# Performance work log

Hardware: AMD Instinct MI355X
Metric: run time of the kernel (lower is better)

Reference implementation:

```python
import jax, jax.numpy as jnp
import numpy as np

L = 44                      # num_lods
IMG = 178                   # output image side
HASH_SIZE = 1 << 10         # codebook_bitwidth = 10
PRIME = np.uint32(2654435761)
RES = np.round(16.0 * (128.0 / 16.0) ** (np.arange(L) / (L - 1.0))).astype(np.int32)
DENSE = (RES + 1) ** 2 <= HASH_SIZE            # dense level if it fits in 2^10 entries
SIZES = np.where(DENSE, (RES + 1) ** 2, HASH_SIZE).astype(np.int32)
OFFS = np.concatenate([[0], np.cumsum(SIZES)[:-1]]).astype(np.int32)
TOTAL = int(SIZES.sum())    # 38584 shared codebook entries (latent_dim = 1)


def setup_inputs() -> dict:
    key = jax.random.key(0)
    k = jax.random.split(key, 5)
    B, N = 16, IMG * IMG
    x = jax.random.uniform(k[0], (B, N, 2), dtype=jnp.float32)            # 2D coords in [0,1]
    codebook = 0.1 * jax.random.normal(k[1], (B, TOTAL, 1), jnp.float32)  # feature_std=0.1
    w1 = jax.random.normal(k[2], (B, 16, L), jnp.float32) / np.sqrt(L)
    w2 = jax.random.normal(k[3], (B, 16, 16), jnp.float32) / 4.0
    w3 = jax.random.normal(k[4], (B, 3, 16), jnp.float32) / 4.0
    return {"x": x, "codebook": codebook, "w1": w1, "w2": w2, "w3": w3}


def _grid_lookup(x, codebook):
    """Multi-LOD hashed 2D grid bilinear lookup. x:[B,N,2], codebook:[B,T,1] -> [B,N,L]."""
    B, N, _ = x.shape
    res_f = jnp.asarray(RES, jnp.float32)
    res_i = jnp.asarray(RES)
    scaled = x[:, :, None, :] * res_f[None, None, :, None]          # [B,N,L,2]
    base = jnp.floor(scaled)
    frac = scaled - base
    base = base.astype(jnp.int32)
    corners = jnp.array([[0, 0], [0, 1], [1, 0], [1, 1]], jnp.int32)  # [4,2]
    c = base[:, :, :, None, :] + corners[None, None, None]          # [B,N,L,4,2]
    c = jnp.minimum(c, res_i[None, None, :, None, None])
    cx, cy = c[..., 0], c[..., 1]
    dense_idx = cy * (res_i + 1)[None, None, :, None] + cx          # row-major dense index
    h = (cx.astype(jnp.uint32) ^ (cy.astype(jnp.uint32) * PRIME)) % jnp.uint32(HASH_SIZE)
    idx = jnp.where(jnp.asarray(DENSE)[None, None, :, None], dense_idx, h.astype(jnp.int32))
    idx = idx + jnp.asarray(OFFS)[None, None, :, None]              # [B,N,L,4] into shared table
    vals = jnp.take_along_axis(codebook[:, :, 0], idx.reshape(B, -1), axis=1).reshape(B, N, L, 4)
    fr = frac[:, :, :, None, :]                                     # [B,N,L,1,2]
    w = jnp.where(corners[None, None, None] == 1, fr, 1.0 - fr).prod(-1)  # bilinear wts [B,N,L,4]
    return (vals * w).sum(-1)                                       # [B,N,L]


def reference(x, codebook, w1, w2, w3):
    feats = _grid_lookup(x, codebook)                               # [B,N,44] ('cat' multiscale)
    h = jax.nn.relu(jnp.einsum('bnl,bhl->bnh', feats, w1))          # per-sample hypernet weights
    h = jax.nn.relu(jnp.einsum('bnh,bkh->bnk', h, w2))
    rgb = jax.nn.sigmoid(jnp.einsum('bnk,bck->bnc', h, w3))         # [B,N,3]
    return rgb.reshape(x.shape[0], IMG, IMG, 3)
```

## Files before the change

kernel.cpp:

```cpp
#include <hip/hip_runtime.h>
#include <math.h>

#define NLEV 44
#define NDENSE 15
#define IMG 178
#define NPTS (IMG*IMG)
#define HASH_SIZE 1024
#define PRIME 2654435761u
#define BLOCK 1024
#define PTS_PER_BLOCK (2*BLOCK)

typedef __attribute__((ext_vector_type(2))) float f32x2;

struct LevelParams {
    int res[NLEV];
    int offs[NLEV];
    int total;
};

#define PKFMA_S(acc, a, b) \
    asm("v_pk_fma_f32 %0, %1, %2, %0" : "+v"(acc) : "v"(a), "s"(b))

__global__ __launch_bounds__(1024) void transpose_w1(const float* __restrict__ w1,
                                                     float* __restrict__ w1t) {
    const int b = blockIdx.x;
    const int i = threadIdx.x;
    if (i < 16 * NLEV) {
        const int l = i >> 4, o = i & 15;
        w1t[(size_t)b * 16 * NLEV + i] = w1[(size_t)b * 16 * NLEV + o * NLEV + l];
    }
}

template<int L0, int CNT, bool TP>
__device__ __forceinline__ void dense_group(
    const LevelParams& lp, const float* __restrict__ sCB,
    const float* __restrict__ w1b,
    float2 xy0, float2 xy1, f32x2* __restrict__ h1a, f32x2* __restrict__ h1b)
{
    float v[2][CNT][4];
    float fr[2][CNT][2];
#pragma unroll
    for (int i = 0; i < CNT; ++i) {
        const int l = L0 + i;
        const int res = lp.res[l];
        const int st  = res + 1;
        const int off = lp.offs[l];
        const float rf = (float)res;
#pragma unroll
        for (int p = 0; p < 2; ++p) {
            const float2 xy = p ? xy1 : xy0;
            const float sx = xy.x * rf, sy = xy.y * rf;
            const int ix0 = (int)sx, iy0 = (int)sy;
            fr[p][i][0] = sx - (float)ix0;
            fr[p][i][1] = sy - (float)iy0;
            const int r0 = off + iy0 * st + ix0;
            v[p][i][0] = sCB[r0];
            v[p][i][1] = sCB[r0 + 1];
            v[p][i][2] = sCB[r0 + st];
            v[p][i][3] = sCB[r0 + st + 1];
        }
    }
#pragma unroll
    for (int i = 0; i < CNT; ++i) {
        const int l = L0 + i;
        f32x2 wlv[8];
        if constexpr (TP) {
            const f32x2* wp = (const f32x2*)(w1b + l * 16);
#pragma unroll
            for (int j = 0; j < 8; ++j) wlv[j] = wp[j];
        } else {
#pragma unroll
            for (int j = 0; j < 8; ++j) {
                wlv[j].x = w1b[(2 * j) * NLEV + l];
                wlv[j].y = w1b[(2 * j + 1) * NLEV + l];
            }
        }
#pragma unroll
        for (int p = 0; p < 2; ++p) {
            f32x2* h1 = p ? h1b : h1a;
            const float vx0 = fmaf(fr[p][i][0], v[p][i][1] - v[p][i][0], v[p][i][0]);
            const float vx1 = fmaf(fr[p][i][0], v[p][i][3] - v[p][i][2], v[p][i][2]);
            const float feat = fmaf(fr[p][i][1], vx1 - vx0, vx0);
            f32x2 f2; f2.x = feat; f2.y = feat;
#pragma unroll
            for (int j = 0; j < 8; ++j) PKFMA_S(h1[j], f2, wlv[j]);
        }
    }
}

template<int L0, int CNT, bool TP>
__device__ __forceinline__ void hash_group(
    const LevelParams& lp, const float* __restrict__ sCB,
    const float* __restrict__ w1b,
    float2 xy0, float2 xy1, f32x2* __restrict__ h1a, f32x2* __restrict__ h1b)
{
    float v[2][CNT][4];
    float fr[2][CNT][2];
#pragma unroll
    for (int i = 0; i < CNT; ++i) {
        const int l = L0 + i;
        const int off = lp.offs[l];
        const float rf = (float)lp.res[l];
#pragma unroll
        for (int p = 0; p < 2; ++p) {
            const float2 xy = p ? xy1 : xy0;
            const float sx = xy.x * rf, sy = xy.y * rf;
            const int ix0 = (int)sx, iy0 = (int)sy;
            fr[p][i][0] = sx - (float)ix0;
            fr[p][i][1] = sy - (float)iy0;
            const unsigned px0 = (unsigned)ix0, px1 = px0 + 1u;
            const unsigned py0 = (unsigned)iy0 * PRIME, py1 = py0 + PRIME;
            const int i00 = (int)((px0 ^ py0) & (HASH_SIZE - 1));
            const int i01 = (int)((px0 ^ py1) & (HASH_SIZE - 1));
            const int i10 = (int)((px1 ^ py0) & (HASH_SIZE - 1));
            const int i11 = (int)((px1 ^ py1) & (HASH_SIZE - 1));
            v[p][i][0] = sCB[off + i00];
            v[p][i][1] = sCB[off + i10];
            v[p][i][2] = sCB[off + i01];
            v[p][i][3] = sCB[off + i11];
        }
    }
#pragma unroll
    for (int i = 0; i < CNT; ++i) {
        const int l = L0 + i;
        f32x2 wlv[8];
        if constexpr (TP) {
            const f32x2* wp = (const f32x2*)(w1b + l * 16);
#pragma unroll
            for (int j = 0; j < 8; ++j) wlv[j] = wp[j];
        } else {
#pragma unroll
            for (int j = 0; j < 8; ++j) {
                wlv[j].x = w1b[(2 * j) * NLEV + l];
                wlv[j].y = w1b[(2 * j + 1) * NLEV + l];
            }
        }
#pragma unroll
        for (int p = 0; p < 2; ++p) {
            f32x2* h1 = p ? h1b : h1a;
            const float vx0 = fmaf(fr[p][i][0], v[p][i][1] - v[p][i][0], v[p][i][0]);
            const float vx1 = fmaf(fr[p][i][0], v[p][i][3] - v[p][i][2], v[p][i][2]);
            const float feat = fmaf(fr[p][i][1], vx1 - vx0, vx0);
            f32x2 f2; f2.x = feat; f2.y = feat;
#pragma unroll
            for (int j = 0; j < 8; ++j) PKFMA_S(h1[j], f2, wlv[j]);
        }
    }
}

template<bool TP>
__global__ __launch_bounds__(BLOCK) void shacira_kernel(
    const float* __restrict__ x, const float* __restrict__ codebook,
    const float* __restrict__ w1, const float* __restrict__ w1t,
    const float* __restrict__ w2, const float* __restrict__ w3,
    float* __restrict__ out, LevelParams lp)
{
    extern __shared__ float sCB[];
    const int total = lp.total;
    const int tid = threadIdx.x;
    const int b = blockIdx.y;

    {
        const float* cbg = codebook + (size_t)b * total;
        const float4* src = (const float4*)cbg;
        float4* dst = (float4*)sCB;
        const int n4 = total >> 2;
        for (int i = tid; i < n4; i += BLOCK) dst[i] = src[i];
        for (int i = (n4 << 2) + tid; i < total; i += BLOCK) sCB[i] = cbg[i];
    }
    __syncthreads();

    const float* w1b = TP ? (w1t + (size_t)b * 16 * NLEV) : (w1 + (size_t)b * 16 * NLEV);
    const float* w2b = w2 + (size_t)b * 256;
    const float* w3b = w3 + (size_t)b * 48;

    const int n0 = blockIdx.x * PTS_PER_BLOCK + tid;
    const int n1 = n0 + BLOCK;
    const bool valid0 = n0 < NPTS;
    const bool valid1 = n1 < NPTS;
    const float2* xg = (const float2*)x + (size_t)b * NPTS;
    float2 xy0 = valid0 ? xg[n0] : make_float2(0.f, 0.f);
    float2 xy1 = valid1 ? xg[n1] : make_float2(0.f, 0.f);

    f32x2 h1a[8], h1b[8];
#pragma unroll
    for (int j = 0; j < 8; ++j) {
        h1a[j].x = 0.f; h1a[j].y = 0.f;
        h1b[j].x = 0.f; h1b[j].y = 0.f;
    }

    dense_group<0, 4, TP>(lp, sCB, w1b, xy0, xy1, h1a, h1b);
    dense_group<4, 4, TP>(lp, sCB, w1b, xy0, xy1, h1a, h1b);
    dense_group<8, 4, TP>(lp, sCB, w1b, xy0, xy1, h1a, h1b);
    dense_group<12, 3, TP>(lp, sCB, w1b, xy0, xy1, h1a, h1b);
    hash_group<15, 4, TP>(lp, sCB, w1b, xy0, xy1, h1a, h1b);
    hash_group<19, 4, TP>(lp, sCB, w1b, xy0, xy1, h1a, h1b);
    hash_group<23, 4, TP>(lp, sCB, w1b, xy0, xy1, h1a, h1b);
    hash_group<27, 4, TP>(lp, sCB, w1b, xy0, xy1, h1a, h1b);
    hash_group<31, 4, TP>(lp, sCB, w1b, xy0, xy1, h1a, h1b);
    hash_group<35, 4, TP>(lp, sCB, w1b, xy0, xy1, h1a, h1b);
    hash_group<39, 4, TP>(lp, sCB, w1b, xy0, xy1, h1a, h1b);
    hash_group<43, 1, TP>(lp, sCB, w1b, xy0, xy1, h1a, h1b);

    auto mlp = [&](f32x2* h1, int n, bool valid) {
        if (!valid) return;
#pragma unroll
        for (int j = 0; j < 8; ++j) {
            h1[j].x = fmaxf(h1[j].x, 0.f);
            h1[j].y = fmaxf(h1[j].y, 0.f);
        }
        float h2[16];
#pragma unroll
        for (int o = 0; o < 16; ++o) {
            const f32x2* w2v = (const f32x2*)(w2b + o * 16);
            f32x2 acc; acc.x = 0.f; acc.y = 0.f;
#pragma unroll
            for (int k = 0; k < 8; ++k) PKFMA_S(acc, h1[k], w2v[k]);
            h2[o] = fmaxf(acc.x + acc.y, 0.f);
        }
        f32x2 h2v[8];
#pragma unroll
        for (int j = 0; j < 8; ++j) { h2v[j].x = h2[2 * j]; h2v[j].y = h2[2 * j + 1]; }
        float rgb[3];
#pragma unroll
        for (int c = 0; c < 3; ++c) {
            const f32x2* w3v = (const f32x2*)(w3b + c * 16);
            f32x2 acc; acc.x = 0.f; acc.y = 0.f;
#pragma unroll
            for (int k = 0; k < 8; ++k) PKFMA_S(acc, h2v[k], w3v[k]);
            rgb[c] = 1.f / (1.f + expf(-(acc.x + acc.y)));
        }
        float* op = out + ((size_t)b * NPTS + n) * 3;
        op[0] = rgb[0]; op[1] = rgb[1]; op[2] = rgb[2];
    };
    mlp(h1a, n0, valid0);
    mlp(h1b, n1, valid1);
}

extern "C" void kernel_launch(void* const* d_in, const int* in_sizes, int n_in,
                              void* d_out, int out_size, void* d_ws, size_t ws_size,
                              hipStream_t stream) {
    const float* x        = (const float*)d_in[0];
    const float* codebook = (const float*)d_in[1];
    const float* w1       = (const float*)d_in[2];
    const float* w2       = (const float*)d_in[3];
    const float* w3       = (const float*)d_in[4];
    float* out = (float*)d_out;

    const int B = in_sizes[0] / (NPTS * 2);

    LevelParams lp;
    int off = 0;
    for (int l = 0; l < NLEV; ++l) {
        const double r = 16.0 * pow(128.0 / 16.0, (double)l / (double)(NLEV - 1));
        const int res = (int)llrint(r);
        lp.res[l] = res;
        lp.offs[l] = off;
        const int sz = ((long long)(res + 1) * (res + 1) <= HASH_SIZE)
                           ? (res + 1) * (res + 1) : HASH_SIZE;
        off += sz;
    }
    lp.total = off;

    const size_t smemBytes = (size_t)lp.total * 4;
    const size_t w1tBytes = (size_t)B * 16 * NLEV * 4;
    const bool tp = ws_size >= w1tBytes;

    dim3 grid((NPTS + PTS_PER_BLOCK - 1) / PTS_PER_BLOCK, B);
    if (tp) {
        transpose_w1<<<dim3(B), dim3(1024), 0, stream>>>(w1, (float*)d_ws);
        hipFuncSetAttribute((const void*)shacira_kernel<true>,
                            hipFuncAttributeMaxDynamicSharedMemorySize, (int)smemBytes);
        shacira_kernel<true><<<grid, dim3(BLOCK), smemBytes, stream>>>(
            x, codebook, w1, (const float*)d_ws, w2, w3, out, lp);
    } else {
        hipFuncSetAttribute((const void*)shacira_kernel<false>,
                            hipFuncAttributeMaxDynamicSharedMemorySize, (int)smemBytes);
        shacira_kernel<false><<<grid, dim3(BLOCK), smemBytes, stream>>>(
            x, codebook, w1, (const float*)0, w2, w3, out, lp);
    }
}
```

Before: 39.98 us.

## Keep only first 36 levels in LDS, gather last 8 hash levels from global

Shrinks the per-block shared-memory codebook copy to the first 36 levels and reads the last 8 hashed levels directly from global memory (served by L2). The aim is to cut the staging copy and LDS footprint, which could allow more resident blocks per CU. In exchange, the random gathers for the finest levels become global loads with much higher latency than LDS reads.

```diff
diff --git a/kernel.cpp b/kernel.cpp
--- a/kernel.cpp
+++ b/kernel.cpp
@@ -3,6 +3,7 @@
 
 #define NLEV 44
 #define NDENSE 15
+#define NLDS 36
 #define IMG 178
 #define NPTS (IMG*IMG)
 #define HASH_SIZE 1024
@@ -16,6 +17,7 @@
     int res[NLEV];
     int offs[NLEV];
     int total;
+    int ldsTotal;
 };
 
 #define PKFMA_S(acc, a, b) \
@@ -28,6 +30,40 @@
     if (i < 16 * NLEV) {
         const int l = i >> 4, o = i & 15;
         w1t[(size_t)b * 16 * NLEV + i] = w1[(size_t)b * 16 * NLEV + o * NLEV + l];
+    }
+}
+
+template<int CNT, bool TP>
+__device__ __forceinline__ void consume_group(
+    int L0, const float* __restrict__ w1b,
+    const float v[2][CNT][4], const float fr[2][CNT][2],
+    f32x2* __restrict__ h1a, f32x2* __restrict__ h1b)
+{
+#pragma unroll
+    for (int i = 0; i < CNT; ++i) {
+        const int l = L0 + i;
+        f32x2 wlv[8];
+        if constexpr (TP) {
+            const f32x2* wp = (const f32x2*)(w1b + l * 16);
+#pragma unroll
+            for (int j = 0; j < 8; ++j) wlv[j] = wp[j];
+        } else {
+#pragma unroll
+            for (int j = 0; j < 8; ++j) {
+                wlv[j].x = w1b[(2 * j) * NLEV + l];
+                wlv[j].y = w1b[(2 * j + 1) * NLEV + l];
+            }
+        }
+#pragma unroll
+        for (int p = 0; p < 2; ++p) {
+            f32x2* h1 = p ? h1b : h1a;
+            const float vx0 = fmaf(fr[p][i][0], v[p][i][1] - v[p][i][0], v[p][i][0]);
+            const float vx1 = fmaf(fr[p][i][0], v[p][i][3] - v[p][i][2], v[p][i][2]);
+            const float feat = fmaf(fr[p][i][1], vx1 - vx0, vx0);
+            f32x2 f2; f2.x = feat; f2.y = feat;
+#pragma unroll
+            for (int j = 0; j < 8; ++j) PKFMA_S(h1[j], f2, wlv[j]);
+        }
     }
 }
 
@@ -60,38 +96,13 @@
             v[p][i][3] = sCB[r0 + st + 1];
         }
     }
-#pragma unroll
-    for (int i = 0; i < CNT; ++i) {
-        const int l = L0 + i;
-        f32x2 wlv[8];
-        if constexpr (TP) {
-            const f32x2* wp = (const f32x2*)(w1b + l * 16);
-#pragma unroll
-            for (int j = 0; j < 8; ++j) wlv[j] = wp[j];
-        } else {
-#pragma unroll
-            for (int j = 0; j < 8; ++j) {
-                wlv[j].x = w1b[(2 * j) * NLEV + l];
-                wlv[j].y = w1b[(2 * j + 1) * NLEV + l];
-            }
-        }
-#pragma unroll
-        for (int p = 0; p < 2; ++p) {
-            f32x2* h1 = p ? h1b : h1a;
-            const float vx0 = fmaf(fr[p][i][0], v[p][i][1] - v[p][i][0], v[p][i][0]);
-            const float vx1 = fmaf(fr[p][i][0], v[p][i][3] - v[p][i][2], v[p][i][2]);
-            const float feat = fmaf(fr[p][i][1], vx1 - vx0, vx0);
-            f32x2 f2; f2.x = feat; f2.y = feat;
-#pragma unroll
-            for (int j = 0; j < 8; ++j) PKFMA_S(h1[j], f2, wlv[j]);
-        }
-    }
-}
-
-template<int L0, int CNT, bool TP>
+    consume_group<CNT, TP>(L0, w1b, v, fr, h1a, h1b);
+}
+
+template<int L0, int CNT, bool TP, bool GLB>
 __device__ __forceinline__ void hash_group(
     const LevelParams& lp, const float* __restrict__ sCB,
-    const float* __restrict__ w1b,
+    const float* __restrict__ cbg, const float* __restrict__ w1b,
     float2 xy0, float2 xy1, f32x2* __restrict__ h1a, f32x2* __restrict__ h1b)
 {
     float v[2][CNT][4];
@@ -114,38 +125,14 @@
             const int i01 = (int)((px0 ^ py1) & (HASH_SIZE - 1));
             const int i10 = (int)((px1 ^ py0) & (HASH_SIZE - 1));
             const int i11 = (int)((px1 ^ py1) & (HASH_SIZE - 1));
-            v[p][i][0] = sCB[off + i00];
-            v[p][i][1] = sCB[off + i10];
-            v[p][i][2] = sCB[off + i01];
-            v[p][i][3] = sCB[off + i11];
-        }
-    }
-#pragma unroll
-    for (int i = 0; i < CNT; ++i) {
-        const int l = L0 + i;
-        f32x2 wlv[8];
-        if constexpr (TP) {
-            const f32x2* wp = (const f32x2*)(w1b + l * 16);
-#pragma unroll
-            for (int j = 0; j < 8; ++j) wlv[j] = wp[j];
-        } else {
-#pragma unroll
-            for (int j = 0; j < 8; ++j) {
-                wlv[j].x = w1b[(2 * j) * NLEV + l];
-                wlv[j].y = w1b[(2 * j + 1) * NLEV + l];
-            }
-        }
-#pragma unroll
-        for (int p = 0; p < 2; ++p) {
-            f32x2* h1 = p ? h1b : h1a;
-            const float vx0 = fmaf(fr[p][i][0], v[p][i][1] - v[p][i][0], v[p][i][0]);
-            const float vx1 = fmaf(fr[p][i][0], v[p][i][3] - v[p][i][2], v[p][i][2]);
-            const float feat = fmaf(fr[p][i][1], vx1 - vx0, vx0);
-            f32x2 f2; f2.x = feat; f2.y = feat;
-#pragma unroll
-            for (int j = 0; j < 8; ++j) PKFMA_S(h1[j], f2, wlv[j]);
-        }
-    }
+            const float* src = GLB ? (cbg + off) : (sCB + off);
+            v[p][i][0] = src[i00];
+            v[p][i][1] = src[i10];
+            v[p][i][2] = src[i01];
+            v[p][i][3] = src[i11];
+        }
+    }
+    consume_group<CNT, TP>(L0, w1b, v, fr, h1a, h1b);
 }
 
 template<bool TP>
@@ -156,17 +143,17 @@
     float* __restrict__ out, LevelParams lp)
 {
     extern __shared__ float sCB[];
-    const int total = lp.total;
     const int tid = threadIdx.x;
     const int b = blockIdx.y;
+    const float* cbg = codebook + (size_t)b * lp.total;
 
     {
-        const float* cbg = codebook + (size_t)b * total;
+        const int ldsTotal = lp.ldsTotal;
         const float4* src = (const float4*)cbg;
         float4* dst = (float4*)sCB;
-        const int n4 = total >> 2;
+        const int n4 = ldsTotal >> 2;
         for (int i = tid; i < n4; i += BLOCK) dst[i] = src[i];
-        for (int i = (n4 << 2) + tid; i < total; i += BLOCK) sCB[i] = cbg[i];
+        for (int i = (n4 << 2) + tid; i < ldsTotal; i += BLOCK) sCB[i] = cbg[i];
     }
     __syncthreads();
 
@@ -193,14 +180,14 @@
     dense_group<4, 4, TP>(lp, sCB, w1b, xy0, xy1, h1a, h1b);
     dense_group<8, 4, TP>(lp, sCB, w1b, xy0, xy1, h1a, h1b);
     dense_group<12, 3, TP>(lp, sCB, w1b, xy0, xy1, h1a, h1b);
-    hash_group<15, 4, TP>(lp, sCB, w1b, xy0, xy1, h1a, h1b);
-    hash_group<19, 4, TP>(lp, sCB, w1b, xy0, xy1, h1a, h1b);
-    hash_group<23, 4, TP>(lp, sCB, w1b, xy0, xy1, h1a, h1b);
-    hash_group<27, 4, TP>(lp, sCB, w1b, xy0, xy1, h1a, h1b);
-    hash_group<31, 4, TP>(lp, sCB, w1b, xy0, xy1, h1a, h1b);
-    hash_group<35, 4, TP>(lp, sCB, w1b, xy0, xy1, h1a, h1b);
-    hash_group<39, 4, TP>(lp, sCB, w1b, xy0, xy1, h1a, h1b);
-    hash_group<43, 1, TP>(lp, sCB, w1b, xy0, xy1, h1a, h1b);
+    hash_group<15, 4, TP, false>(lp, sCB, cbg, w1b, xy0, xy1, h1a, h1b);
+    hash_group<19, 4, TP, false>(lp, sCB, cbg, w1b, xy0, xy1, h1a, h1b);
+    hash_group<23, 4, TP, false>(lp, sCB, cbg, w1b, xy0, xy1, h1a, h1b);
+    hash_group<27, 4, TP, false>(lp, sCB, cbg, w1b, xy0, xy1, h1a, h1b);
+    hash_group<31, 4, TP, false>(lp, sCB, cbg, w1b, xy0, xy1, h1a, h1b);
+    hash_group<35, 1, TP, false>(lp, sCB, cbg, w1b, xy0, xy1, h1a, h1b);
+    hash_group<36, 4, TP, true>(lp, sCB, cbg, w1b, xy0, xy1, h1a, h1b);
+    hash_group<40, 4, TP, true>(lp, sCB, cbg, w1b, xy0, xy1, h1a, h1b);
 
     auto mlp = [&](f32x2* h1, int n, bool valid) {
         if (!valid) return;
@@ -261,8 +248,9 @@
         off += sz;
     }
     lp.total = off;
-
-    const size_t smemBytes = (size_t)lp.total * 4;
+    lp.ldsTotal = lp.offs[NLDS];
+
+    const size_t smemBytes = (size_t)lp.ldsTotal * 4;
     const size_t w1tBytes = (size_t)B * 16 * NLEV * 4;
     const bool tp = ws_size >= w1tBytes;
 
```

New measurement: 44.85 us. 12.2% more time.
